# Kernel tuning notes

Measured on AMD Instinct MI355X. Metric: run time of the kernel, lower is better.

The kernel has to match this reference:

```python
import jax, jax.numpy as jnp
import numpy as np

BN_EPS = 1e-5

def _bn(x, g, b):
    # BatchNorm1d, training-mode batch statistics
    mu = x.mean(axis=0)
    var = x.var(axis=0)
    return g * (x - mu) / jnp.sqrt(var + BN_EPS) + b

def setup_inputs() -> dict:
    key = jax.random.key(0)
    ks = jax.random.split(key, 10)
    B2, D_in, D1, DIMS, C = 16384, 1024, 512, 256, 40
    B = B2 // 2
    def w(k, shape, fan_in):
        return jax.random.normal(k, shape, jnp.float32) / np.float32(np.sqrt(fan_in))
    return {
        "lufeat": jax.random.normal(ks[0], (B2, D_in), jnp.float32),
        "llabel": jax.random.randint(ks[1], (B,), 0, C),
        "W1": w(ks[2], (D_in, D1), D_in), "b1": jnp.zeros(D1, jnp.float32),
        "W2": w(ks[3], (D1, DIMS), D1), "b2": jnp.zeros(DIMS, jnp.float32),
        "W3": w(ks[4], (DIMS + C, 256), DIMS + C), "b3": jnp.zeros(256, jnp.float32),
        "W4": w(ks[5], (256, 64), 256), "b4": jnp.zeros(64, jnp.float32),
        "W5": w(ks[6], (64, 1), 64), "b5": jnp.zeros(1, jnp.float32),
        "g1": jnp.ones(256, jnp.float32), "be1": jnp.zeros(256, jnp.float32),
        "g2": jnp.ones(64, jnp.float32), "be2": jnp.zeros(64, jnp.float32),
        "mbank0": jax.random.normal(ks[7], (C, DIMS), jnp.float32),
        "start0": jnp.zeros(C, jnp.float32),
    }

def reference(lufeat, llabel, W1, b1, W2, b2, W3, b3, W4, b4, W5, b5,
              g1, be1, g2, be2, mbank0, start0):
    B = lufeat.shape[0] // 2
    h = (lufeat @ W1 + b1) @ W2 + b2            # [2B, dims]
    h = h / jnp.linalg.norm(h, axis=1, keepdims=True)
    lfeat, ufeat = h[:B], h[B:]

    # Sequential per-sample memory-bank scatter/EMA update (detached feats)
    lf_sg = jax.lax.stop_gradient(lfeat)
    def step(carry, xs):
        start, mbank = carry
        lab, feat = xs
        row = jnp.where(start[lab] == 0, feat, 0.9 * mbank[lab] + 0.1 * feat)
        return (start.at[lab].set(1.0), mbank.at[lab].set(row)), None
    (_, mbank), _ = jax.lax.scan(step, (start0, mbank0), (llabel, lf_sg))
    mbank = jax.lax.stop_gradient(mbank)

    # cdist retrieval: [B, C] euclidean distances
    lm = jnp.linalg.norm(lfeat[:, None, :] - mbank[None, :, :], axis=-1)
    lscores = lm.min(axis=-1)
    um = jnp.linalg.norm(ufeat[:, None, :] - mbank[None, :, :], axis=-1)

    uf = jnp.concatenate([ufeat, um], axis=-1)   # [B, dims + C]
    u = jax.nn.relu(_bn(uf @ W3 + b3, g1, be1))
    u = jax.nn.relu(_bn(u @ W4 + b4, g2, be2))   # dropout = identity (eval)
    uscores = u @ W5 + b5                        # [B, 1]
    return lscores, uscores, mbank
```

## Files before the change

### kernel.cpp

```cpp
#include <hip/hip_runtime.h>
#include <hip/hip_bf16.h>
#include <stdint.h>

typedef __attribute__((ext_vector_type(4))) float f32x4;
typedef __attribute__((ext_vector_type(8))) short s16x8;
typedef __attribute__((ext_vector_type(4))) unsigned short u16x4;
typedef __attribute__((ext_vector_type(4))) int i32x4;

#define B2T 16384
#define BH 8192
#define DIN 1024
#define DD1 512
#define DIMS 256
#define NC 40
#define CAPS 2048

__device__ __forceinline__ unsigned short f2b(float f) {
  unsigned int u = __builtin_bit_cast(unsigned int, f);
  u += 0x7FFFu + ((u >> 16) & 1u);
  return (unsigned short)(u >> 16);
}

__device__ __forceinline__ float b2f(unsigned short u) {
  return __builtin_bit_cast(float, ((unsigned int)u) << 16);
}

__device__ __forceinline__ void gload16(const void* g, void* l) {
  __builtin_amdgcn_global_load_lds(
      (const __attribute__((address_space(1))) void*)g,
      (__attribute__((address_space(3))) void*)l, 16, 0, 0);
}

__global__ __launch_bounds__(256) void prep_all(const float* __restrict__ W1,
                                                const float* __restrict__ W2,
                                                const float* __restrict__ b1,
                                                const float* __restrict__ b2,
                                                const float* __restrict__ W3,
                                                const float* __restrict__ W4,
                                                unsigned short* __restrict__ WeffT,
                                                float* __restrict__ beff,
                                                unsigned short* __restrict__ W3T,
                                                unsigned short* __restrict__ W4T,
                                                float* __restrict__ statz) {
  __shared__ float W1s[32][36];
  __shared__ float W2sT[32][36];
  int b = blockIdx.x, t = threadIdx.x;
  if (b < 256) {
    int k0 = (b & 31) * 32, n0 = (b >> 5) * 32;
    int nn = t & 31, kq = t >> 5;
    f32x4 acc = (f32x4){0.f, 0.f, 0.f, 0.f};
    for (int j0 = 0; j0 < DD1; j0 += 32) {
#pragma unroll
      for (int i = 0; i < 4; ++i) {
        int idx = t + 256 * i;
        int kk = idx >> 5, jj = idx & 31;
        W1s[kk][jj] = W1[(size_t)(k0 + kk) * DD1 + j0 + jj];
        W2sT[jj][kk] = W2[(size_t)(j0 + kk) * DIMS + n0 + jj];
      }
      __syncthreads();
#pragma unroll
      for (int jj4 = 0; jj4 < 8; ++jj4) {
        f32x4 w2 = *(const f32x4*)&W2sT[nn][jj4 * 4];
        f32x4 w1_0 = *(const f32x4*)&W1s[kq * 4 + 0][jj4 * 4];
        f32x4 w1_1 = *(const f32x4*)&W1s[kq * 4 + 1][jj4 * 4];
        f32x4 w1_2 = *(const f32x4*)&W1s[kq * 4 + 2][jj4 * 4];
        f32x4 w1_3 = *(const f32x4*)&W1s[kq * 4 + 3][jj4 * 4];
        acc[0] += w1_0[0] * w2[0] + w1_0[1] * w2[1] + w1_0[2] * w2[2] + w1_0[3] * w2[3];
        acc[1] += w1_1[0] * w2[0] + w1_1[1] * w2[1] + w1_1[2] * w2[2] + w1_1[3] * w2[3];
        acc[2] += w1_2[0] * w2[0] + w1_2[1] * w2[1] + w1_2[2] * w2[2] + w1_2[3] * w2[3];
        acc[3] += w1_3[0] * w2[0] + w1_3[1] * w2[1] + w1_3[2] * w2[2] + w1_3[3] * w2[3];
      }
      __syncthreads();
    }
    u16x4 pk = {f2b(acc[0]), f2b(acc[1]), f2b(acc[2]), f2b(acc[3])};
    *(u16x4*)(WeffT + (size_t)(n0 + nn) * DIN + k0 + kq * 4) = pk;
  } else if (b == 256) {
    float a0 = 0.f, a1 = 0.f, a2 = 0.f, a3 = 0.f, a4 = 0.f, a5 = 0.f, a6 = 0.f, a7 = 0.f;
    for (int j = 0; j < DD1; j += 8) {
      a0 += b1[j + 0] * W2[(size_t)(j + 0) * DIMS + t];
      a1 += b1[j + 1] * W2[(size_t)(j + 1) * DIMS + t];
      a2 += b1[j + 2] * W2[(size_t)(j + 2) * DIMS + t];
      a3 += b1[j + 3] * W2[(size_t)(j + 3) * DIMS + t];
      a4 += b1[j + 4] * W2[(size_t)(j + 4) * DIMS + t];
      a5 += b1[j + 5] * W2[(size_t)(j + 5) * DIMS + t];
      a6 += b1[j + 6] * W2[(size_t)(j + 6) * DIMS + t];
      a7 += b1[j + 7] * W2[(size_t)(j + 7) * DIMS + t];
    }
    beff[t] = b2[t] + (((a0 + a1) + (a2 + a3)) + ((a4 + a5) + (a6 + a7)));
  } else if (b < 577) {
    int idx = (b - 257) * 256 + t;
    int n = idx / 320, k = idx - n * 320;
    float v = (k < 296) ? W3[(size_t)k * 256 + n] : 0.0f;
    W3T[(size_t)n * 320 + k] = f2b(v);
  } else if (b < 641) {
    int idx = (b - 577) * 256 + t;
    int n = idx >> 8, k = idx & 255;
    W4T[(size_t)n * 256 + k] = f2b(W4[(size_t)k * 64 + n]);
  } else {
    for (int i = t; i < 640; i += 256) statz[i] = 0.0f;
  }
}

template <int AMODE, int NB, int MI, int CW, int EPI, int K, int TPB>
__global__ __launch_bounds__(TPB) void gemm_core(
    const void* __restrict__ Aptr, int lda, const unsigned short* __restrict__ BT,
    const float* __restrict__ bias, float* __restrict__ C, int ldc,
    float* __restrict__ sums, float* __restrict__ ssqs,
    const float* __restrict__ bnsum, const float* __restrict__ bnssq,
    const float* __restrict__ bng, const float* __restrict__ bnbe,
    unsigned short* __restrict__ uf) {
  constexpr int NW = TPB / 64;
  constexpr int RG = NW / CW;
  constexpr int AR = RG * MI * 16;
  constexpr int ACH = AR * 8;
  constexpr int ABN = (ACH + TPB - 1) / TPB;
  constexpr int BBN = NB * 8 / TPB;
  constexpr int BBUF = NB * 128;
  constexpr int ALOADS = (AMODE == 1) ? ABN : 2 * ABN;
  constexpr bool UNIF = (ACH >= TPB);
  __shared__ __align__(16) short A_s[2][AR][72];
  __shared__ __align__(16) char B_s[2 * BBUF];
  __shared__ float rs[CW][AR];
  __shared__ float bsc_s[(AMODE == 2) ? 256 : 1];
  __shared__ float bsh_s[(AMODE == 2) ? 256 : 1];
  int t = threadIdx.x;
  int m0 = blockIdx.x * AR;
  int w = t >> 6, lane = t & 63, q = lane >> 4, ln = lane & 15;
  f32x4 acc[MI][4];
#pragma unroll
  for (int mi = 0; mi < MI; ++mi)
#pragma unroll
    for (int ni = 0; ni < 4; ++ni) acc[mi][ni] = (f32x4){0.f, 0.f, 0.f, 0.f};

  f32x4 pa0[ABN][2], pa1[ABN][2];
  s16x8 pab0[ABN], pab1[ABN];

  auto issue = [&](int kbase, f32x4 (&paX)[ABN][2], s16x8 (&pabX)[ABN]) {
    if (ACH >= TPB || t < ACH) {
#pragma unroll
      for (int i = 0; i < ABN; ++i) {
        int ch = t + TPB * i, row = ch >> 3, kp = (ch & 7) * 8;
        if constexpr (AMODE == 1) {
          const unsigned short* A = (const unsigned short*)Aptr;
          pabX[i] = *(const s16x8*)(A + (size_t)(m0 + row) * lda + kbase + kp);
        } else {
          const float* A = (const float*)Aptr;
          const f32x4* src = (const f32x4*)(A + (size_t)(m0 + row) * lda + kbase + kp);
          paX[i][0] = src[0];
          paX[i][1] = src[1];
        }
      }
    }
  };

  auto gloadB = [&](int kbase, int bufi) {
#pragma unroll
    for (int i = 0; i < BBN; ++i) {
      int ch = t + TPB * i;
      int n = ch >> 3, j = ch & 7;
      int ksw = (j ^ (n & 7)) * 8;
      gload16(BT + (size_t)n * K + kbase + ksw,
              B_s + bufi * BBUF + (w * 64 + TPB * i) * 16);
    }
  };

  auto stage = [&](int kk, int bufi, f32x4 (&paX)[ABN][2], s16x8 (&pabX)[ABN]) {
    if (ACH >= TPB || t < ACH) {
#pragma unroll
      for (int i = 0; i < ABN; ++i) {
        int ch = t + TPB * i, row = ch >> 3, kp = (ch & 7) * 8;
        if constexpr (AMODE == 1) {
          *(s16x8*)&A_s[bufi][row][kp] = pabX[i];
        } else {
          f32x4 v0 = paX[i][0], v1 = paX[i][1];
          if constexpr (AMODE == 2) {
            float vv[8] = {v0[0], v0[1], v0[2], v0[3], v1[0], v1[1], v1[2], v1[3]};
#pragma unroll
            for (int j = 0; j < 8; ++j) {
              int f = kk + kp + j;
              vv[j] = fmaxf(vv[j] * bsc_s[f] + bsh_s[f], 0.0f);
            }
            v0 = (f32x4){vv[0], vv[1], vv[2], vv[3]};
            v1 = (f32x4){vv[4], vv[5], vv[6], vv[7]};
          }
          s16x8 p;
          p[0] = (short)f2b(v0[0]); p[1] = (short)f2b(v0[1]);
          p[2] = (short)f2b(v0[2]); p[3] = (short)f2b(v0[3]);
          p[4] = (short)f2b(v1[0]); p[5] = (short)f2b(v1[1]);
          p[6] = (short)f2b(v1[2]); p[7] = (short)f2b(v1[3]);
          *(s16x8*)&A_s[bufi][row][kp] = p;
        }
      }
    }
  };

  auto compute = [&](int cur) {
#pragma unroll
    for (int k32 = 0; k32 < 64; k32 += 32) {
      s16x8 af[MI];
      int ab = (w / CW) * MI * 16;
#pragma unroll
      for (int mi = 0; mi < MI; ++mi)
        af[mi] = *(const s16x8*)&A_s[cur][ab + mi * 16 + ln][k32 + q * 8];
      int nb0 = (w % CW) * 64;
#pragma unroll
      for (int ni = 0; ni < 4; ++ni) {
        int brow = nb0 + ni * 16 + ln;
        int bb = (brow * 128 + (k32 + q * 8) * 2) ^ ((brow & 7) << 4);
        s16x8 bfr = *(const s16x8*)(B_s + cur * BBUF + bb);
#pragma unroll
        for (int mi = 0; mi < MI; ++mi)
          acc[mi][ni] = __builtin_amdgcn_mfma_f32_16x16x32_bf16(af[mi], bfr, acc[mi][ni], 0, 0, 0);
      }
    }
  };

  auto kbar = [&](bool keepA) {
    if constexpr (UNIF) {
      if (keepA)
        asm volatile("s_waitcnt vmcnt(%0) lgkmcnt(0)" ::"n"(ALOADS) : "memory");
      else
        asm volatile("s_waitcnt vmcnt(0) lgkmcnt(0)" ::: "memory");
      __builtin_amdgcn_s_barrier();
      __builtin_amdgcn_sched_barrier(0);
    } else {
      __syncthreads();
    }
  };

  if constexpr (AMODE == 2) {
    if (t < 256) {
      float mu = bnsum[t] * (1.0f / 8192.0f);
      float var = bnssq[t] * (1.0f / 8192.0f) - mu * mu;
      float sc = bng[t] * rsqrtf(var + 1e-5f);
      bsc_s[t] = sc;
      bsh_s[t] = bnbe[t] - mu * sc;
    }
    __syncthreads();
  }

  const int nst = K >> 6;
  issue(0, pa0, pab0);
  gloadB(0, 0);
  __builtin_amdgcn_sched_barrier(0);
  if (nst > 1) issue(64, pa1, pab1);
  stage(0, 0, pa0, pab0);
  kbar(nst > 1);

  for (int s = 0; s < nst; s += 2) {
    if (s + 1 < nst) gloadB((s + 1) << 6, 1);
    __builtin_amdgcn_sched_barrier(0);
    if (s + 2 < nst) issue((s + 2) << 6, pa0, pab0);
    compute(0);
    if (s + 1 < nst) stage((s + 1) << 6, 1, pa1, pab1);
    kbar(s + 2 < nst);
    if (s + 1 < nst) {
      if (s + 2 < nst) gloadB((s + 2) << 6, 0);
      __builtin_amdgcn_sched_barrier(0);
      if (s + 3 < nst) issue((s + 3) << 6, pa1, pab1);
      compute(1);
      if (s + 2 < nst) stage((s + 2) << 6, 0, pa0, pab0);
      kbar(s + 3 < nst);
    }
  }

  float v[MI][4][4];
#pragma unroll
  for (int mi = 0; mi < MI; ++mi)
#pragma unroll
    for (int ni = 0; ni < 4; ++ni) {
      float bv = bias[(w % CW) * 64 + ni * 16 + ln];
#pragma unroll
      for (int r = 0; r < 4; ++r) v[mi][ni][r] = acc[mi][ni][r] + bv;
    }

  if constexpr (EPI == 1) {
    float p[MI][4];
#pragma unroll
    for (int mi = 0; mi < MI; ++mi)
#pragma unroll
      for (int r = 0; r < 4; ++r) {
        float s = v[mi][0][r] * v[mi][0][r] + v[mi][1][r] * v[mi][1][r] +
                  v[mi][2][r] * v[mi][2][r] + v[mi][3][r] * v[mi][3][r];
        s += __shfl_xor(s, 1); s += __shfl_xor(s, 2);
        s += __shfl_xor(s, 4); s += __shfl_xor(s, 8);
        p[mi][r] = s;
      }
    if (ln == 0) {
#pragma unroll
      for (int mi = 0; mi < MI; ++mi)
#pragma unroll
        for (int r = 0; r < 4; ++r)
          rs[w % CW][(w / CW) * MI * 16 + mi * 16 + q * 4 + r] = p[mi][r];
    }
    __syncthreads();
    if (t < AR) {
      float s = rs[0][t];
#pragma unroll
      for (int i = 1; i < CW; ++i) s += rs[i][t];
      rs[0][t] = rsqrtf(s);
    }
    __syncthreads();
#pragma unroll
    for (int mi = 0; mi < MI; ++mi)
#pragma unroll
      for (int r = 0; r < 4; ++r) {
        int ribf = (w / CW) * MI * 16 + mi * 16 + q * 4 + r;
        float inv = rs[0][ribf];
        int grow = m0 + ribf;
#pragma unroll
        for (int ni = 0; ni < 4; ++ni) {
          int col = (w % CW) * 64 + ni * 16 + ln;
          float nv = v[mi][ni][r] * inv;
          if (grow < BH)
            C[(size_t)grow * ldc + col] = nv;
          else
            uf[(size_t)(grow - BH) * 320 + col] = f2b(nv);
        }
      }
  } else {
#pragma unroll
    for (int mi = 0; mi < MI; ++mi)
#pragma unroll
      for (int ni = 0; ni < 4; ++ni)
#pragma unroll
        for (int r = 0; r < 4; ++r) {
          int grow = m0 + (w / CW) * MI * 16 + mi * 16 + q * 4 + r;
          int col = (w % CW) * 64 + ni * 16 + ln;
          C[(size_t)grow * ldc + col] = v[mi][ni][r];
        }
    if constexpr (EPI == 2 || EPI == 3) {
#pragma unroll
      for (int ni = 0; ni < 4; ++ni) {
        float s = 0.f, s2 = 0.f;
#pragma unroll
        for (int mi = 0; mi < MI; ++mi)
#pragma unroll
          for (int r = 0; r < 4; ++r) {
            float x = v[mi][ni][r];
            s += x; s2 += x * x;
          }
        s += __shfl_xor(s, 16); s += __shfl_xor(s, 32);
        s2 += __shfl_xor(s2, 16); s2 += __shfl_xor(s2, 32);
        if (q == 0) {
          int col = (w % CW) * 64 + ni * 16 + ln;
          atomicAdd(&sums[col], s);
          atomicAdd(&ssqs[col], s2);
        }
      }
    }
  }
}

__global__ __launch_bounds__(256) void bank_kernel(const int* __restrict__ llabel,
                                                   const float* __restrict__ Hn,
                                                   const float* __restrict__ mbank0,
                                                   const float* __restrict__ start0,
                                                   float* __restrict__ mbank_out,
                                                   float* __restrict__ msq) {
  __shared__ i32x4 lab4[BH / 4];
  __shared__ int idx_s[CAPS];
  __shared__ int wcnt[4];
  __shared__ float red[4];
  int t = threadIdx.x, c = blockIdx.x;
  int w = t >> 6, lane = t & 63;

  for (int i = t; i < BH / 4; i += 256) lab4[i] = ((const i32x4*)llabel)[i];
  __syncthreads();
  const int* lab_s = (const int*)lab4;

  int base0 = w * (BH / 4);
  int cnt = 0;
  for (int b = 0; b < BH / 4; b += 64)
    cnt += (int)__popcll(__ballot(lab_s[base0 + b + lane] == c));
  if (lane == 0) wcnt[w] = cnt;
  __syncthreads();
  int off = 0;
#pragma unroll
  for (int i = 0; i < 4; ++i)
    if (i < w) off += wcnt[i];
  int Ktot = wcnt[0] + wcnt[1] + wcnt[2] + wcnt[3];

  int running = off;
  for (int b = 0; b < BH / 4; b += 64) {
    bool hit = lab_s[base0 + b + lane] == c;
    unsigned long long mk = __ballot(hit);
    if (hit) {
      int pos = running + (int)__popcll(mk & ((1ull << lane) - 1ull));
      if (pos < CAPS) idx_s[pos] = base0 + b + lane;
    }
    running += (int)__popcll(mk);
  }
  __syncthreads();
  int K = Ktot < CAPS ? Ktot : CAPS;

  const float l09 = -0.15200309344504997f;
  bool fresh = (start0[c] == 0.0f);
  float out;
  if (K == 0) {
    out = mbank0[(size_t)c * DIMS + t];
  } else {
    float a0 = 0.f, a1 = 0.f, a2 = 0.f, a3 = 0.f, a4 = 0.f, a5 = 0.f, a6 = 0.f, a7 = 0.f;
    float w0fold = fresh ? exp2f((float)K * l09) : 0.f;
    int m = 0;
    for (; m + 8 <= K; m += 8) {
      float e = (float)(K - 1 - m);
      float wa = 0.1f * exp2f(e * l09) + (m == 0 ? w0fold : 0.f);
      a0 += wa * Hn[(size_t)idx_s[m + 0] * DIMS + t];
      a1 += 0.1f * exp2f((e - 1.f) * l09) * Hn[(size_t)idx_s[m + 1] * DIMS + t];
      a2 += 0.1f * exp2f((e - 2.f) * l09) * Hn[(size_t)idx_s[m + 2] * DIMS + t];
      a3 += 0.1f * exp2f((e - 3.f) * l09) * Hn[(size_t)idx_s[m + 3] * DIMS + t];
      a4 += 0.1f * exp2f((e - 4.f) * l09) * Hn[(size_t)idx_s[m + 4] * DIMS + t];
      a5 += 0.1f * exp2f((e - 5.f) * l09) * Hn[(size_t)idx_s[m + 5] * DIMS + t];
      a6 += 0.1f * exp2f((e - 6.f) * l09) * Hn[(size_t)idx_s[m + 6] * DIMS + t];
      a7 += 0.1f * exp2f((e - 7.f) * l09) * Hn[(size_t)idx_s[m + 7] * DIMS + t];
    }
    for (; m < K; ++m) {
      float wa = 0.1f * exp2f((float)(K - 1 - m) * l09) + (m == 0 ? w0fold : 0.f);
      a0 += wa * Hn[(size_t)idx_s[m] * DIMS + t];
    }
    float acc = ((a0 + a1) + (a2 + a3)) + ((a4 + a5) + (a6 + a7));
    float base_v = fresh ? 0.f : exp2f((float)K * l09) * mbank0[(size_t)c * DIMS + t];
    out = acc + base_v;
  }
  mbank_out[(size_t)c * DIMS + t] = out;
  float vv = out * out;
#pragma unroll
  for (int o = 32; o; o >>= 1) vv += __shfl_xor(vv, o);
  if ((t & 63) == 0) red[t >> 6] = vv;
  __syncthreads();
  if (t == 0) msq[c] = (red[0] + red[1]) + (red[2] + red[3]);
}

__global__ __launch_bounds__(256) void dist_kernel(const float* __restrict__ Hn,
                                                   const float* __restrict__ mbank,
                                                   const float* __restrict__ msq,
                                                   float* __restrict__ lscores,
                                                   unsigned short* __restrict__ uf) {
  __shared__ float Ms[NC][260];
  __shared__ float Hs[32][260];
  __shared__ float msq_s[NC];
  int t = threadIdx.x;
  int r0 = blockIdx.x * 32;
  for (int e = t; e < NC * 64; e += 256) {
    int i = e >> 6, d0 = (e & 63) * 4;
    *(f32x4*)&Ms[i][d0] = *(const f32x4*)(mbank + (size_t)i * DIMS + d0);
  }
  if (r0 < BH) {
    for (int e = t; e < 32 * 64; e += 256) {
      int i = e >> 6, d0 = (e & 63) * 4;
      *(f32x4*)&Hs[i][d0] = *(const f32x4*)(Hn + (size_t)(r0 + i) * DIMS + d0);
    }
  } else {
    for (int e = t; e < 32 * 32; e += 256) {
      int i = e >> 5, d0 = (e & 31) * 8;
      s16x8 vb = *(const s16x8*)(uf + (size_t)(r0 - BH + i) * 320 + d0);
#pragma unroll
      for (int j = 0; j < 8; ++j) Hs[i][d0 + j] = b2f((unsigned short)vb[j]);
    }
  }
  if (t < NC) msq_s[t] = msq[t];
  __syncthreads();
  int r = t >> 3, c0 = (t & 7) * 5;
  float g0 = 0, g1 = 0, g2 = 0, g3 = 0, g4 = 0;
  for (int d = 0; d < DIMS; d += 4) {
    f32x4 f = *(const f32x4*)&Hs[r][d];
    f32x4 m0v = *(const f32x4*)&Ms[c0 + 0][d];
    f32x4 m1v = *(const f32x4*)&Ms[c0 + 1][d];
    f32x4 m2v = *(const f32x4*)&Ms[c0 + 2][d];
    f32x4 m3v = *(const f32x4*)&Ms[c0 + 3][d];
    f32x4 m4v = *(const f32x4*)&Ms[c0 + 4][d];
    g0 += f[0] * m0v[0] + f[1] * m0v[1] + f[2] * m0v[2] + f[3] * m0v[3];
    g1 += f[0] * m1v[0] + f[1] * m1v[1] + f[2] * m1v[2] + f[3] * m1v[3];
    g2 += f[0] * m2v[0] + f[1] * m2v[1] + f[2] * m2v[2] + f[3] * m2v[3];
    g3 += f[0] * m3v[0] + f[1] * m3v[1] + f[2] * m3v[2] + f[3] * m3v[3];
    g4 += f[0] * m4v[0] + f[1] * m4v[1] + f[2] * m4v[2] + f[3] * m4v[3];
  }
  int row = r0 + r;
  float d2[5];
  d2[0] = 1.0f + msq_s[c0 + 0] - 2.0f * g0;
  d2[1] = 1.0f + msq_s[c0 + 1] - 2.0f * g1;
  d2[2] = 1.0f + msq_s[c0 + 2] - 2.0f * g2;
  d2[3] = 1.0f + msq_s[c0 + 3] - 2.0f * g3;
  d2[4] = 1.0f + msq_s[c0 + 4] - 2.0f * g4;
  if (row < BH) {
    float mn = fminf(fminf(fminf(d2[0], d2[1]), fminf(d2[2], d2[3])), d2[4]);
    mn = fminf(mn, __shfl_xor(mn, 1, 8));
    mn = fminf(mn, __shfl_xor(mn, 2, 8));
    mn = fminf(mn, __shfl_xor(mn, 4, 8));
    if ((t & 7) == 0) lscores[row] = sqrtf(fmaxf(mn, 0.0f));
  } else {
    unsigned short* dst = uf + (size_t)(row - BH) * 320 + 256 + c0;
#pragma unroll
    for (int qq = 0; qq < 5; ++qq) dst[qq] = f2b(sqrtf(fmaxf(d2[qq], 0.0f)));
  }
}

__global__ __launch_bounds__(256) void uscore_bn(const float* __restrict__ y2,
                                                 const float* __restrict__ sums2,
                                                 const float* __restrict__ ssqs2,
                                                 const float* __restrict__ g2,
                                                 const float* __restrict__ be2,
                                                 const float* __restrict__ W5,
                                                 const float* __restrict__ b5,
                                                 float* __restrict__ out) {
  int t = threadIdx.x;
  int wv = t >> 6, lane = t & 63;
  int row = blockIdx.x * 4 + wv;
  float mu = sums2[lane] * (1.0f / 8192.0f);
  float var = ssqs2[lane] * (1.0f / 8192.0f) - mu * mu;
  float sc = g2[lane] * rsqrtf(var + 1e-5f);
  float sh = be2[lane] - mu * sc;
  float v = fmaxf(y2[(size_t)row * 64 + lane] * sc + sh, 0.0f) * W5[lane];
#pragma unroll
  for (int o = 32; o; o >>= 1) v += __shfl_xor(v, o);
  if (lane == 0) out[row] = v + b5[0];
}

extern "C" void kernel_launch(void* const* d_in, const int* in_sizes, int n_in,
                              void* d_out, int out_size, void* d_ws, size_t ws_size,
                              hipStream_t stream) {
  const float* lufeat = (const float*)d_in[0];
  const int* llabel = (const int*)d_in[1];
  const float* W1 = (const float*)d_in[2];
  const float* b1 = (const float*)d_in[3];
  const float* W2 = (const float*)d_in[4];
  const float* b2 = (const float*)d_in[5];
  const float* W3 = (const float*)d_in[6];
  const float* b3 = (const float*)d_in[7];
  const float* W4 = (const float*)d_in[8];
  const float* b4 = (const float*)d_in[9];
  const float* W5 = (const float*)d_in[10];
  const float* b5 = (const float*)d_in[11];
  const float* g1 = (const float*)d_in[12];
  const float* be1 = (const float*)d_in[13];
  const float* g2 = (const float*)d_in[14];
  const float* be2 = (const float*)d_in[15];
  const float* mbank0 = (const float*)d_in[16];
  const float* start0 = (const float*)d_in[17];

  char* ws = (char*)d_ws;
  unsigned short* WeffT = (unsigned short*)(ws + 0);
  float* Hraw = (float*)(ws + 524288);
  float* ybuf = (float*)(ws + 524288);
  float* y2 = (float*)(ws + 8912896);
  unsigned short* uf = (unsigned short*)(ws + 17301504);
  unsigned short* W3T = (unsigned short*)(ws + 22544384);
  unsigned short* W4T = (unsigned short*)(ws + 22708224);
  float* beff = (float*)(ws + 22740992);
  float* sums1 = (float*)(ws + 22742016);
  float* ssq1 = sums1 + 256;
  float* sums2 = ssq1 + 256;
  float* ssq2 = sums2 + 64;
  float* msq = (float*)(ws + 22744576);

  float* lscores = (float*)d_out;
  float* uscores = lscores + 8192;
  float* mbank = uscores + 8192;

  prep_all<<<642, 256, 0, stream>>>(W1, W2, b1, b2, W3, W4, WeffT, beff, W3T, W4T, sums1);
  gemm_core<0, 256, 2, 4, 1, 1024, 256><<<512, 256, 0, stream>>>(
      lufeat, 1024, WeffT, beff, Hraw, 256,
      nullptr, nullptr, nullptr, nullptr, nullptr, nullptr, uf);
  bank_kernel<<<NC, 256, 0, stream>>>(llabel, Hraw, mbank0, start0, mbank, msq);
  dist_kernel<<<512, 256, 0, stream>>>(Hraw, mbank, msq, lscores, uf);
  gemm_core<1, 256, 1, 4, 2, 320, 512><<<256, 512, 0, stream>>>(
      uf, 320, W3T, b3, ybuf, 256,
      sums1, ssq1, nullptr, nullptr, nullptr, nullptr, nullptr);
  gemm_core<2, 64, 1, 1, 3, 256, 256><<<128, 256, 0, stream>>>(
      ybuf, 256, W4T, b4, y2, 64,
      sums2, ssq2, sums1, ssq1, g1, be1, nullptr);
  uscore_bn<<<2048, 256, 0, stream>>>(y2, sums2, ssq2, g2, be2, W5, b5, uscores);
}
```

Before: 236.3 us.

## Pre-convert input to bf16 and use a DMA-staged first GEMM; split bank kernel

The prep kernel now converts the 16384x1024 fp32 input to bf16 in workspace. A new dedicated first GEMM kernel loads A and B tiles straight into swizzled LDS with global_load_lds and double buffering, then applies the row-normalisation epilogue. The memory-bank kernel is split four ways across feature columns (160 blocks), accumulating row norms with atomics into a zeroed msq. This adds a separate full pass over the input (fp32 read plus bf16 write) to allow cheaper DMA loads in the GEMM, and trades that against better bank-kernel parallelism.

After: 238.2 us. Within noise of the previous version (+0.8%).

```diff
diff --git a/kernel.cpp b/kernel.cpp
--- a/kernel.cpp
+++ b/kernel.cpp
@@ -31,7 +31,9 @@
       (__attribute__((address_space(3))) void*)l, 16, 0, 0);
 }
 
-__global__ __launch_bounds__(256) void prep_all(const float* __restrict__ W1,
+__global__ __launch_bounds__(256) void prep_all(const float* __restrict__ lufeat,
+                                                unsigned short* __restrict__ lufeatH,
+                                                const float* __restrict__ W1,
                                                 const float* __restrict__ W2,
                                                 const float* __restrict__ b1,
                                                 const float* __restrict__ b2,
@@ -45,8 +47,22 @@
   __shared__ float W1s[32][36];
   __shared__ float W2sT[32][36];
   int b = blockIdx.x, t = threadIdx.x;
-  if (b < 256) {
-    int k0 = (b & 31) * 32, n0 = (b >> 5) * 32;
+  if (b < 1024) {
+#pragma unroll
+    for (int i = 0; i < 8; ++i) {
+      int idx = b * 16384 + i * 2048 + t * 8;
+      f32x4 v0 = *(const f32x4*)(lufeat + idx);
+      f32x4 v1 = *(const f32x4*)(lufeat + idx + 4);
+      s16x8 p;
+      p[0] = (short)f2b(v0[0]); p[1] = (short)f2b(v0[1]);
+      p[2] = (short)f2b(v0[2]); p[3] = (short)f2b(v0[3]);
+      p[4] = (short)f2b(v1[0]); p[5] = (short)f2b(v1[1]);
+      p[6] = (short)f2b(v1[2]); p[7] = (short)f2b(v1[3]);
+      *(s16x8*)(lufeatH + idx) = p;
+    }
+  } else if (b < 1280) {
+    int bb = b - 1024;
+    int k0 = (bb & 31) * 32, n0 = (bb >> 5) * 32;
     int nn = t & 31, kq = t >> 5;
     f32x4 acc = (f32x4){0.f, 0.f, 0.f, 0.f};
     for (int j0 = 0; j0 < DD1; j0 += 32) {
@@ -74,7 +90,7 @@
     }
     u16x4 pk = {f2b(acc[0]), f2b(acc[1]), f2b(acc[2]), f2b(acc[3])};
     *(u16x4*)(WeffT + (size_t)(n0 + nn) * DIN + k0 + kq * 4) = pk;
-  } else if (b == 256) {
+  } else if (b == 1280) {
     float a0 = 0.f, a1 = 0.f, a2 = 0.f, a3 = 0.f, a4 = 0.f, a5 = 0.f, a6 = 0.f, a7 = 0.f;
     for (int j = 0; j < DD1; j += 8) {
       a0 += b1[j + 0] * W2[(size_t)(j + 0) * DIMS + t];
@@ -87,18 +103,129 @@
       a7 += b1[j + 7] * W2[(size_t)(j + 7) * DIMS + t];
     }
     beff[t] = b2[t] + (((a0 + a1) + (a2 + a3)) + ((a4 + a5) + (a6 + a7)));
-  } else if (b < 577) {
-    int idx = (b - 257) * 256 + t;
+  } else if (b < 1601) {
+    int idx = (b - 1281) * 256 + t;
     int n = idx / 320, k = idx - n * 320;
     float v = (k < 296) ? W3[(size_t)k * 256 + n] : 0.0f;
     W3T[(size_t)n * 320 + k] = f2b(v);
-  } else if (b < 641) {
-    int idx = (b - 577) * 256 + t;
+  } else if (b < 1665) {
+    int idx = (b - 1601) * 256 + t;
     int n = idx >> 8, k = idx & 255;
     W4T[(size_t)n * 256 + k] = f2b(W4[(size_t)k * 64 + n]);
   } else {
-    for (int i = t; i < 640; i += 256) statz[i] = 0.0f;
-  }
+    for (int i = t; i < 680; i += 256) statz[i] = 0.0f;
+  }
+}
+
+__global__ __launch_bounds__(256) void gemm1_dma(
+    const unsigned short* __restrict__ AH, const unsigned short* __restrict__ BT,
+    const float* __restrict__ bias, float* __restrict__ C,
+    unsigned short* __restrict__ uf) {
+  __shared__ __align__(16) char A_s[2][4096];
+  __shared__ __align__(16) char B_s[2][32768];
+  __shared__ float rs[4][32];
+  int t = threadIdx.x, m0 = blockIdx.x * 32;
+  int w = t >> 6, lane = t & 63, q = lane >> 4, ln = lane & 15;
+  f32x4 acc[2][4];
+#pragma unroll
+  for (int mi = 0; mi < 2; ++mi)
+#pragma unroll
+    for (int ni = 0; ni < 4; ++ni) acc[mi][ni] = (f32x4){0.f, 0.f, 0.f, 0.f};
+
+  auto dma = [&](int s, int bufi) {
+    int kb = s * 64;
+    {
+      int row = t >> 3, j = t & 7;
+      gload16(AH + (size_t)(m0 + row) * 1024 + kb + ((j ^ (row & 7)) * 8),
+              A_s[bufi] + t * 16);
+    }
+#pragma unroll
+    for (int i = 0; i < 8; ++i) {
+      int ch = t + 256 * i, n = ch >> 3, j = ch & 7;
+      gload16(BT + (size_t)n * 1024 + kb + ((j ^ (n & 7)) * 8),
+              B_s[bufi] + (w * 64 + 256 * i) * 16);
+    }
+  };
+
+  auto compute = [&](int bufi) {
+#pragma unroll
+    for (int k32 = 0; k32 < 64; k32 += 32) {
+      int koff = (k32 + q * 8) * 2;
+      s16x8 af[2];
+#pragma unroll
+      for (int mi = 0; mi < 2; ++mi) {
+        int row = mi * 16 + ln;
+        af[mi] = *(const s16x8*)(A_s[bufi] + ((row * 128 + koff) ^ ((row & 7) << 4)));
+      }
+      int nb0 = w * 64;
+#pragma unroll
+      for (int ni = 0; ni < 4; ++ni) {
+        int brow = nb0 + ni * 16 + ln;
+        s16x8 bfr = *(const s16x8*)(B_s[bufi] + ((brow * 128 + koff) ^ ((brow & 7) << 4)));
+#pragma unroll
+        for (int mi = 0; mi < 2; ++mi)
+          acc[mi][ni] = __builtin_amdgcn_mfma_f32_16x16x32_bf16(af[mi], bfr, acc[mi][ni], 0, 0, 0);
+      }
+    }
+  };
+
+  dma(0, 0);
+  __syncthreads();
+  for (int s = 0; s < 16; ++s) {
+    if (s + 1 < 16) dma(s + 1, (s + 1) & 1);
+    compute(s & 1);
+    __syncthreads();
+  }
+
+  float v[2][4][4];
+#pragma unroll
+  for (int mi = 0; mi < 2; ++mi)
+#pragma unroll
+    for (int ni = 0; ni < 4; ++ni) {
+      float bv = bias[w * 64 + ni * 16 + ln];
+#pragma unroll
+      for (int r = 0; r < 4; ++r) v[mi][ni][r] = acc[mi][ni][r] + bv;
+    }
+  float p[2][4];
+#pragma unroll
+  for (int mi = 0; mi < 2; ++mi)
+#pragma unroll
+    for (int r = 0; r < 4; ++r) {
+      float s = v[mi][0][r] * v[mi][0][r] + v[mi][1][r] * v[mi][1][r] +
+                v[mi][2][r] * v[mi][2][r] + v[mi][3][r] * v[mi][3][r];
+      s += __shfl_xor(s, 1); s += __shfl_xor(s, 2);
+      s += __shfl_xor(s, 4); s += __shfl_xor(s, 8);
+      p[mi][r] = s;
+    }
+  if (ln == 0) {
+#pragma unroll
+    for (int mi = 0; mi < 2; ++mi)
+#pragma unroll
+      for (int r = 0; r < 4; ++r) rs[w][mi * 16 + q * 4 + r] = p[mi][r];
+  }
+  __syncthreads();
+  if (t < 32) {
+    float s = rs[0][t] + rs[1][t] + rs[2][t] + rs[3][t];
+    rs[0][t] = rsqrtf(s);
+  }
+  __syncthreads();
+#pragma unroll
+  for (int mi = 0; mi < 2; ++mi)
+#pragma unroll
+    for (int r = 0; r < 4; ++r) {
+      int ribf = mi * 16 + q * 4 + r;
+      float inv = rs[0][ribf];
+      int grow = m0 + ribf;
+#pragma unroll
+      for (int ni = 0; ni < 4; ++ni) {
+        int col = w * 64 + ni * 16 + ln;
+        float nv = v[mi][ni][r] * inv;
+        if (grow < BH)
+          C[(size_t)grow * DIMS + col] = nv;
+        else
+          uf[(size_t)(grow - BH) * 320 + col] = f2b(nv);
+      }
+    }
 }
 
 template <int AMODE, int NB, int MI, int CW, int EPI, int K, int TPB>
@@ -274,79 +401,33 @@
       for (int r = 0; r < 4; ++r) v[mi][ni][r] = acc[mi][ni][r] + bv;
     }
 
-  if constexpr (EPI == 1) {
-    float p[MI][4];
-#pragma unroll
-    for (int mi = 0; mi < MI; ++mi)
+#pragma unroll
+  for (int mi = 0; mi < MI; ++mi)
+#pragma unroll
+    for (int ni = 0; ni < 4; ++ni)
 #pragma unroll
       for (int r = 0; r < 4; ++r) {
-        float s = v[mi][0][r] * v[mi][0][r] + v[mi][1][r] * v[mi][1][r] +
-                  v[mi][2][r] * v[mi][2][r] + v[mi][3][r] * v[mi][3][r];
-        s += __shfl_xor(s, 1); s += __shfl_xor(s, 2);
-        s += __shfl_xor(s, 4); s += __shfl_xor(s, 8);
-        p[mi][r] = s;
-      }
-    if (ln == 0) {
+        int grow = m0 + (w / CW) * MI * 16 + mi * 16 + q * 4 + r;
+        int col = (w % CW) * 64 + ni * 16 + ln;
+        C[(size_t)grow * ldc + col] = v[mi][ni][r];
+      }
+  if constexpr (EPI == 2 || EPI == 3) {
+#pragma unroll
+    for (int ni = 0; ni < 4; ++ni) {
+      float s = 0.f, s2 = 0.f;
 #pragma unroll
       for (int mi = 0; mi < MI; ++mi)
 #pragma unroll
-        for (int r = 0; r < 4; ++r)
-          rs[w % CW][(w / CW) * MI * 16 + mi * 16 + q * 4 + r] = p[mi][r];
-    }
-    __syncthreads();
-    if (t < AR) {
-      float s = rs[0][t];
-#pragma unroll
-      for (int i = 1; i < CW; ++i) s += rs[i][t];
-      rs[0][t] = rsqrtf(s);
-    }
-    __syncthreads();
-#pragma unroll
-    for (int mi = 0; mi < MI; ++mi)
-#pragma unroll
-      for (int r = 0; r < 4; ++r) {
-        int ribf = (w / CW) * MI * 16 + mi * 16 + q * 4 + r;
-        float inv = rs[0][ribf];
-        int grow = m0 + ribf;
-#pragma unroll
-        for (int ni = 0; ni < 4; ++ni) {
-          int col = (w % CW) * 64 + ni * 16 + ln;
-          float nv = v[mi][ni][r] * inv;
-          if (grow < BH)
-            C[(size_t)grow * ldc + col] = nv;
-          else
-            uf[(size_t)(grow - BH) * 320 + col] = f2b(nv);
+        for (int r = 0; r < 4; ++r) {
+          float x = v[mi][ni][r];
+          s += x; s2 += x * x;
         }
-      }
-  } else {
-#pragma unroll
-    for (int mi = 0; mi < MI; ++mi)
-#pragma unroll
-      for (int ni = 0; ni < 4; ++ni)
-#pragma unroll
-        for (int r = 0; r < 4; ++r) {
-          int grow = m0 + (w / CW) * MI * 16 + mi * 16 + q * 4 + r;
-          int col = (w % CW) * 64 + ni * 16 + ln;
-          C[(size_t)grow * ldc + col] = v[mi][ni][r];
-        }
-    if constexpr (EPI == 2 || EPI == 3) {
-#pragma unroll
-      for (int ni = 0; ni < 4; ++ni) {
-        float s = 0.f, s2 = 0.f;
-#pragma unroll
-        for (int mi = 0; mi < MI; ++mi)
-#pragma unroll
-          for (int r = 0; r < 4; ++r) {
-            float x = v[mi][ni][r];
-            s += x; s2 += x * x;
-          }
-        s += __shfl_xor(s, 16); s += __shfl_xor(s, 32);
-        s2 += __shfl_xor(s2, 16); s2 += __shfl_xor(s2, 32);
-        if (q == 0) {
-          int col = (w % CW) * 64 + ni * 16 + ln;
-          atomicAdd(&sums[col], s);
-          atomicAdd(&ssqs[col], s2);
-        }
+      s += __shfl_xor(s, 16); s += __shfl_xor(s, 32);
+      s2 += __shfl_xor(s2, 16); s2 += __shfl_xor(s2, 32);
+      if (q == 0) {
+        int col = (w % CW) * 64 + ni * 16 + ln;
+        atomicAdd(&sums[col], s);
+        atomicAdd(&ssqs[col], s2);
       }
     }
   }
@@ -360,10 +441,11 @@
                                                    float* __restrict__ msq) {
   __shared__ i32x4 lab4[BH / 4];
   __shared__ int idx_s[CAPS];
+  __shared__ float redp[256];
   __shared__ int wcnt[4];
-  __shared__ float red[4];
-  int t = threadIdx.x, c = blockIdx.x;
+  int t = threadIdx.x, c = blockIdx.x >> 2, dq = blockIdx.x & 3;
   int w = t >> 6, lane = t & 63;
+  const float l09 = -0.15200309344504997f;
 
   for (int i = t; i < BH / 4; i += 256) lab4[i] = ((const i32x4*)llabel)[i];
   __syncthreads();
@@ -380,7 +462,6 @@
   for (int i = 0; i < 4; ++i)
     if (i < w) off += wcnt[i];
   int Ktot = wcnt[0] + wcnt[1] + wcnt[2] + wcnt[3];
-
   int running = off;
   for (int b = 0; b < BH / 4; b += 64) {
     bool hit = lab_s[base0 + b + lane] == c;
@@ -393,43 +474,43 @@
   }
   __syncthreads();
   int K = Ktot < CAPS ? Ktot : CAPS;
-
-  const float l09 = -0.15200309344504997f;
   bool fresh = (start0[c] == 0.0f);
-  float out;
-  if (K == 0) {
-    out = mbank0[(size_t)c * DIMS + t];
-  } else {
-    float a0 = 0.f, a1 = 0.f, a2 = 0.f, a3 = 0.f, a4 = 0.f, a5 = 0.f, a6 = 0.f, a7 = 0.f;
+  int dcol = t & 63, rr = t >> 6;
+  int d = dq * 64 + dcol;
+  float p0 = 0.f, p1 = 0.f, p2 = 0.f, p3 = 0.f;
+  if (K > 0) {
     float w0fold = fresh ? exp2f((float)K * l09) : 0.f;
-    int m = 0;
-    for (; m + 8 <= K; m += 8) {
+    int m = rr;
+    for (; m + 12 < K; m += 16) {
       float e = (float)(K - 1 - m);
       float wa = 0.1f * exp2f(e * l09) + (m == 0 ? w0fold : 0.f);
-      a0 += wa * Hn[(size_t)idx_s[m + 0] * DIMS + t];
-      a1 += 0.1f * exp2f((e - 1.f) * l09) * Hn[(size_t)idx_s[m + 1] * DIMS + t];
-      a2 += 0.1f * exp2f((e - 2.f) * l09) * Hn[(size_t)idx_s[m + 2] * DIMS + t];
-      a3 += 0.1f * exp2f((e - 3.f) * l09) * Hn[(size_t)idx_s[m + 3] * DIMS + t];
-      a4 += 0.1f * exp2f((e - 4.f) * l09) * Hn[(size_t)idx_s[m + 4] * DIMS + t];
-      a5 += 0.1f * exp2f((e - 5.f) * l09) * Hn[(size_t)idx_s[m + 5] * DIMS + t];
-      a6 += 0.1f * exp2f((e - 6.f) * l09) * Hn[(size_t)idx_s[m + 6] * DIMS + t];
-      a7 += 0.1f * exp2f((e - 7.f) * l09) * Hn[(size_t)idx_s[m + 7] * DIMS + t];
-    }
-    for (; m < K; ++m) {
+      p0 += wa * Hn[(size_t)idx_s[m] * DIMS + d];
+      p1 += 0.1f * exp2f((e - 4.f) * l09) * Hn[(size_t)idx_s[m + 4] * DIMS + d];
+      p2 += 0.1f * exp2f((e - 8.f) * l09) * Hn[(size_t)idx_s[m + 8] * DIMS + d];
+      p3 += 0.1f * exp2f((e - 12.f) * l09) * Hn[(size_t)idx_s[m + 12] * DIMS + d];
+    }
+    for (; m < K; m += 4) {
       float wa = 0.1f * exp2f((float)(K - 1 - m) * l09) + (m == 0 ? w0fold : 0.f);
-      a0 += wa * Hn[(size_t)idx_s[m] * DIMS + t];
-    }
-    float acc = ((a0 + a1) + (a2 + a3)) + ((a4 + a5) + (a6 + a7));
-    float base_v = fresh ? 0.f : exp2f((float)K * l09) * mbank0[(size_t)c * DIMS + t];
-    out = acc + base_v;
-  }
-  mbank_out[(size_t)c * DIMS + t] = out;
-  float vv = out * out;
-#pragma unroll
-  for (int o = 32; o; o >>= 1) vv += __shfl_xor(vv, o);
-  if ((t & 63) == 0) red[t >> 6] = vv;
-  __syncthreads();
-  if (t == 0) msq[c] = (red[0] + red[1]) + (red[2] + red[3]);
+      p0 += wa * Hn[(size_t)idx_s[m] * DIMS + d];
+    }
+  }
+  redp[rr * 64 + dcol] = (p0 + p1) + (p2 + p3);
+  __syncthreads();
+  if (t < 64) {
+    int dd = dq * 64 + t;
+    float out;
+    if (K == 0) {
+      out = mbank0[(size_t)c * DIMS + dd];
+    } else {
+      float base_v = fresh ? 0.f : exp2f((float)K * l09) * mbank0[(size_t)c * DIMS + dd];
+      out = ((redp[t] + redp[64 + t]) + (redp[128 + t] + redp[192 + t])) + base_v;
+    }
+    mbank_out[(size_t)c * DIMS + dd] = out;
+    float vv = out * out;
+#pragma unroll
+    for (int o = 32; o; o >>= 1) vv += __shfl_xor(vv, o);
+    if (t == 0) atomicAdd(&msq[c], vv);
+  }
 }
 
 __global__ __launch_bounds__(256) void dist_kernel(const float* __restrict__ Hn,
@@ -553,16 +634,16 @@
   float* sums2 = ssq1 + 256;
   float* ssq2 = sums2 + 64;
   float* msq = (float*)(ws + 22744576);
+  unsigned short* lufeatH = (unsigned short*)(ws + 25165824);
 
   float* lscores = (float*)d_out;
   float* uscores = lscores + 8192;
   float* mbank = uscores + 8192;
 
-  prep_all<<<642, 256, 0, stream>>>(W1, W2, b1, b2, W3, W4, WeffT, beff, W3T, W4T, sums1);
-  gemm_core<0, 256, 2, 4, 1, 1024, 256><<<512, 256, 0, stream>>>(
-      lufeat, 1024, WeffT, beff, Hraw, 256,
-      nullptr, nullptr, nullptr, nullptr, nullptr, nullptr, uf);
-  bank_kernel<<<NC, 256, 0, stream>>>(llabel, Hraw, mbank0, start0, mbank, msq);
+  prep_all<<<1666, 256, 0, stream>>>(lufeat, lufeatH, W1, W2, b1, b2, W3, W4,
+                                     WeffT, beff, W3T, W4T, sums1);
+  gemm1_dma<<<512, 256, 0, stream>>>(lufeatH, WeffT, beff, Hraw, uf);
+  bank_kernel<<<160, 256, 0, stream>>>(llabel, Hraw, mbank0, start0, mbank, msq);
   dist_kernel<<<512, 256, 0, stream>>>(Hraw, mbank, msq, lscores, uf);
   gemm_core<1, 256, 1, 4, 2, 320, 512><<<256, 512, 0, stream>>>(
       uf, 320, W3T, b3, ybuf, 256,
```
